# Optimization experiments

Measured on AMD Instinct MI355X. Metric: run time of the kernel, lower is better.

Reference implementation:

```python
import jax, jax.numpy as jnp
import numpy as np

B, N, F_IN = 2, 768, 10
FEATS = [F_IN, 128, 128, 64]  # DeepSet layer widths
D2 = 2 * FEATS[-1]            # lin2: cat of two broadcasts
H_MLP = 64                    # suffix hidden width
OUT = 1
SCALE = 0.05


def setup_inputs() -> dict:
    key = jax.random.key(0)
    ks = jax.random.split(key, 32)
    d = {"x": jax.random.normal(ks[0], (B, N, F_IN), dtype=jnp.float32)}
    i = 1
    for l, (ci, co) in enumerate(zip(FEATS[:-1], FEATS[1:])):
        d[f"w1_{l}"] = SCALE * jax.random.normal(ks[i], (co, ci), dtype=jnp.float32); i += 1
        d[f"b1_{l}"] = SCALE * jax.random.normal(ks[i], (co,), dtype=jnp.float32); i += 1
        d[f"w2_{l}"] = SCALE * jax.random.normal(ks[i], (co, ci), dtype=jnp.float32); i += 1
        d[f"b2_{l}"] = SCALE * jax.random.normal(ks[i], (co,), dtype=jnp.float32); i += 1
    d["sw0"] = SCALE * jax.random.normal(ks[i], (H_MLP, D2), dtype=jnp.float32); i += 1
    d["sb0"] = SCALE * jax.random.normal(ks[i], (H_MLP,), dtype=jnp.float32); i += 1
    d["sw1"] = SCALE * jax.random.normal(ks[i], (OUT, H_MLP), dtype=jnp.float32); i += 1
    d["sb1"] = SCALE * jax.random.normal(ks[i], (OUT,), dtype=jnp.float32)
    return d


def _deepset_layer(h, w1, b1, w2, b2):
    # h: (B, C, N). layer1(h) + layer2(h - mean_N(h)), both 1x1 convs.
    hm = h - h.mean(axis=2, keepdims=True)
    y = jnp.einsum('oc,bcn->bon', w1, h) + b1[None, :, None]
    y = y + jnp.einsum('oc,bcn->bon', w2, hm) + b2[None, :, None]
    return y


def reference(x, w1_0, b1_0, w2_0, b2_0, w1_1, b1_1, w2_1, b2_1,
              w1_2, b1_2, w2_2, b2_2, sw0, sb0, sw1, sb1):
    h = x.transpose(0, 2, 1)  # (B, F_IN, N)
    h = jax.nn.relu(_deepset_layer(h, w1_0, b1_0, w2_0, b2_0))
    h = jax.nn.relu(_deepset_layer(h, w1_1, b1_1, w2_1, b2_1))
    u = _deepset_layer(h, w1_2, b1_2, w2_2, b2_2)  # (B, f, N), no ReLU after last
    f = u.shape[1]
    # lin2 block: cat(m1, m2) over channels with m1[b,c,i,j]=u[b,c,j],
    # m2[b,c,i,j]=u[b,c,i]. The first 1x1 conv distributes over the concat:
    #   sw0 @ block = sw0[:, :f] @ m1 + sw0[:, f:] @ m2
    p = jnp.einsum('oc,bcn->bon', sw0[:, :f], u)   # contribution broadcast over i
    q = jnp.einsum('oc,bcn->bon', sw0[:, f:], u)   # contribution broadcast over j
    h1 = jax.nn.relu(p[:, :, None, :] + q[:, :, :, None] + sb0[None, :, None, None])  # (B, H, N, N)
    out = jnp.einsum('oc,bcij->boij', sw1, h1) + sb1[None, :, None, None]  # (B, 1, N, N)
    return out
```

## Files before the change

kernel.cpp:

```cpp
#include <hip/hip_runtime.h>

#define BB 2
#define NN 768
#define FIN 10

#define WPQ_OFF 0
#define S1P_OFF 16384
#define S2P_OFF (S1P_OFF + BB*6*128)
#define H1_OFF  (S2P_OFF + BB*12*128)
#define H2_OFF  (H1_OFF + BB*128*NN)
#define PP_OFF  (H2_OFF + BB*128*NN)
#define QQ_OFF  (PP_OFF + BB*64*NN)

__global__ void k_wpq(const float* __restrict__ sw0, const float* __restrict__ w1_2,
                      const float* __restrict__ w2_2, float* __restrict__ wpq)
{
    const int o0 = blockIdx.x * 16, tid = threadIdx.x;
    __shared__ float w2l[64][132];
    __shared__ float sl[16][64];
    for (int idx = tid; idx < 2048; idx += 256) {
        int k = idx >> 5, c4 = (idx & 31) * 4;
        float4 a = *(const float4*)&w1_2[k * 128 + c4];
        float4 b = *(const float4*)&w2_2[k * 128 + c4];
        float4 r = {a.x + b.x, a.y + b.y, a.z + b.z, a.w + b.w};
        *(float4*)&w2l[k][c4] = r;
    }
    for (int idx = tid; idx < 16 * 64; idx += 256) {
        int o = idx >> 6, k = idx & 63;
        int oo = o0 + o;
        sl[o][k] = (oo < 64) ? sw0[oo * 128 + k] : sw0[(oo - 64) * 128 + 64 + k];
    }
    __syncthreads();
    const int tx = tid & 31, ty = tid >> 5;
    float4 a0 = {0, 0, 0, 0}, a1 = {0, 0, 0, 0};
    for (int k = 0; k < 64; ++k) {
        float4 wv = *(const float4*)&w2l[k][tx * 4];
        float s0 = sl[ty * 2][k], s1 = sl[ty * 2 + 1][k];
        a0.x += s0 * wv.x; a0.y += s0 * wv.y; a0.z += s0 * wv.z; a0.w += s0 * wv.w;
        a1.x += s1 * wv.x; a1.y += s1 * wv.y; a1.z += s1 * wv.z; a1.w += s1 * wv.w;
    }
    *(float4*)&wpq[(o0 + ty * 2) * 128 + tx * 4] = a0;
    *(float4*)&wpq[(o0 + ty * 2 + 1) * 128 + tx * 4] = a1;
}

__global__ void k_layer0(const float* __restrict__ x, const float* __restrict__ w1,
                         const float* __restrict__ w2, const float* __restrict__ b1,
                         const float* __restrict__ b2, float* __restrict__ h1,
                         float* __restrict__ s1p)
{
    const int b = blockIdx.x, nblk = blockIdx.y, n0 = nblk * 128, tid = threadIdx.x;
    __shared__ float red[FIN][257];
    __shared__ float mu[FIN];
    __shared__ float xt[FIN][128];
    __shared__ float wl[FIN][128];
    __shared__ float offs[128];
    __shared__ float red2[8][16][33];
    float acc[FIN];
#pragma unroll
    for (int c = 0; c < FIN; ++c) acc[c] = 0.f;
    for (int n = tid; n < NN; n += 256) {
        const float* xp = x + (b * NN + n) * FIN;
#pragma unroll
        for (int c = 0; c < FIN; ++c) acc[c] += xp[c];
    }
#pragma unroll
    for (int c = 0; c < FIN; ++c) red[c][tid] = acc[c];
    __syncthreads();
    for (int s = 128; s > 0; s >>= 1) {
        if (tid < s) {
#pragma unroll
            for (int c = 0; c < FIN; ++c) red[c][tid] += red[c][tid + s];
        }
        __syncthreads();
    }
    if (tid < FIN) mu[tid] = red[tid][0] * (1.f / (float)NN);
    for (int idx = tid; idx < FIN * 128; idx += 256) {
        int n = idx / FIN, c = idx % FIN;
        xt[c][n] = x[(b * NN + n0 + n) * FIN + c];
    }
    for (int idx = tid; idx < FIN * 128; idx += 256) {
        int o = idx / FIN, c = idx % FIN;
        wl[c][o] = w1[o * FIN + c] + w2[o * FIN + c];
    }
    __syncthreads();
    if (tid < 128) {
        float o = b1[tid] + b2[tid];
#pragma unroll
        for (int c = 0; c < FIN; ++c) o -= w2[tid * FIN + c] * mu[c];
        offs[tid] = o;
    }
    __syncthreads();
    const int tx = tid & 31, ty = tid >> 5;
    float4 av[16];
#pragma unroll
    for (int a = 0; a < 16; ++a) {
        float o = offs[ty * 16 + a];
        av[a] = make_float4(o, o, o, o);
    }
#pragma unroll
    for (int c = 0; c < FIN; ++c) {
        float4 xv = *(const float4*)&xt[c][tx * 4];
#pragma unroll
        for (int a = 0; a < 16; ++a) {
            float w = wl[c][ty * 16 + a];
            av[a].x += w * xv.x; av[a].y += w * xv.y;
            av[a].z += w * xv.z; av[a].w += w * xv.w;
        }
    }
#pragma unroll
    for (int a = 0; a < 16; ++a) {
        float4 r = av[a];
        r.x = fmaxf(r.x, 0.f); r.y = fmaxf(r.y, 0.f);
        r.z = fmaxf(r.z, 0.f); r.w = fmaxf(r.w, 0.f);
        *(float4*)&h1[((size_t)(b * 128 + ty * 16 + a)) * NN + n0 + tx * 4] = r;
        red2[ty][a][tx] = r.x + r.y + r.z + r.w;
    }
    __syncthreads();
    if (tid < 128) {
        float s = 0.f;
#pragma unroll
        for (int t = 0; t < 32; ++t) s += red2[tid >> 4][tid & 15][t];
        s1p[(b * 6 + nblk) * 128 + tid] = s;
    }
}

__global__ void k_layer1(const float* __restrict__ h1, const float* __restrict__ w1,
                         const float* __restrict__ b1, const float* __restrict__ w2,
                         const float* __restrict__ b2, const float* __restrict__ s1p,
                         float* __restrict__ h2, float* __restrict__ s2p)
{
    const int b = blockIdx.x, nblk = blockIdx.y, n0 = nblk * 64,
              o0 = blockIdx.z * 64, tid = threadIdx.x;
    __shared__ float hl[128][64];
    __shared__ float wl[64][132];
    __shared__ float mul[128];
    __shared__ float offp[4][64];
    __shared__ float offs[64];
    __shared__ float red[16][4][17];
    if (tid < 128) {
        float s = 0.f;
#pragma unroll
        for (int k = 0; k < 6; ++k) s += s1p[(b * 6 + k) * 128 + tid];
        mul[tid] = s * (1.f / (float)NN);
    }
    for (int idx = tid; idx < 2048; idx += 256) {
        int c = idx >> 4, n4 = (idx & 15) * 4;
        *(float4*)&hl[c][n4] = *(const float4*)&h1[((size_t)(b * 128 + c)) * NN + n0 + n4];
    }
    for (int idx = tid; idx < 2048; idx += 256) {
        int o = idx >> 5, c4 = (idx & 31) * 4;
        float4 a = *(const float4*)&w1[(o0 + o) * 128 + c4];
        float4 bb = *(const float4*)&w2[(o0 + o) * 128 + c4];
        float4 r = {a.x + bb.x, a.y + bb.y, a.z + bb.z, a.w + bb.w};
        *(float4*)&wl[o][c4] = r;
    }
    __syncthreads();
    {
        int o = tid & 63, part = tid >> 6;
        const float* w2r = w2 + (o0 + o) * 128 + part * 32;
        const float* mr = mul + part * 32;
        float p = 0.f;
#pragma unroll
        for (int i = 0; i < 32; ++i) p += w2r[i] * mr[i];
        offp[part][o] = p;
    }
    __syncthreads();
    if (tid < 64)
        offs[tid] = b1[o0 + tid] + b2[o0 + tid]
                  - offp[0][tid] - offp[1][tid] - offp[2][tid] - offp[3][tid];
    __syncthreads();
    const int tx = tid & 15, ty = tid >> 4;
    float4 acc[4];
#pragma unroll
    for (int a = 0; a < 4; ++a) acc[a] = make_float4(0.f, 0.f, 0.f, 0.f);
    for (int c = 0; c < 128; ++c) {
        float4 hv = *(const float4*)&hl[c][tx * 4];
#pragma unroll
        for (int a = 0; a < 4; ++a) {
            float w = wl[ty * 4 + a][c];
            acc[a].x += w * hv.x; acc[a].y += w * hv.y;
            acc[a].z += w * hv.z; acc[a].w += w * hv.w;
        }
    }
#pragma unroll
    for (int a = 0; a < 4; ++a) {
        int o = ty * 4 + a;
        float off = offs[o];
        float4 r = acc[a];
        r.x = fmaxf(r.x + off, 0.f); r.y = fmaxf(r.y + off, 0.f);
        r.z = fmaxf(r.z + off, 0.f); r.w = fmaxf(r.w + off, 0.f);
        *(float4*)&h2[((size_t)(b * 128 + o0 + o)) * NN + n0 + tx * 4] = r;
        red[ty][a][tx] = r.x + r.y + r.z + r.w;
    }
    __syncthreads();
    if (tid < 64) {
        float s = 0.f;
#pragma unroll
        for (int t = 0; t < 16; ++t) s += red[tid >> 2][tid & 3][t];
        s2p[(b * 12 + nblk) * 128 + o0 + tid] = s;
    }
}

__global__ void k_pq(const float* __restrict__ h2, const float* __restrict__ wpq,
                     const float* __restrict__ b1_2, const float* __restrict__ w2_2,
                     const float* __restrict__ b2_2, const float* __restrict__ sw0,
                     const float* __restrict__ sb0, const float* __restrict__ s2p,
                     float* __restrict__ pp, float* __restrict__ qq)
{
    const int b = blockIdx.x, nblk = blockIdx.y, n0 = nblk * 64,
              z = blockIdx.z, o0 = z * 64, tid = threadIdx.x;
    __shared__ float hl[128][64];
    __shared__ float wl[64][132];
    __shared__ float mul[128];
    __shared__ float offp[4][64];
    __shared__ float off2[64];
    __shared__ float bp[4][64];
    __shared__ float bias[64];
    if (tid < 128) {
        float s = 0.f;
#pragma unroll
        for (int k = 0; k < 12; ++k) s += s2p[(b * 12 + k) * 128 + tid];
        mul[tid] = s * (1.f / (float)NN);
    }
    for (int idx = tid; idx < 2048; idx += 256) {
        int c = idx >> 4, n4 = (idx & 15) * 4;
        *(float4*)&hl[c][n4] = *(const float4*)&h2[((size_t)(b * 128 + c)) * NN + n0 + n4];
    }
    for (int idx = tid; idx < 2048; idx += 256) {
        int o = idx >> 5, c4 = (idx & 31) * 4;
        *(float4*)&wl[o][c4] = *(const float4*)&wpq[(o0 + o) * 128 + c4];
    }
    __syncthreads();
    {
        int k = tid & 63, part = tid >> 6;
        const float* w2r = w2_2 + k * 128 + part * 32;
        const float* mr = mul + part * 32;
        float p = 0.f;
#pragma unroll
        for (int i = 0; i < 32; ++i) p += w2r[i] * mr[i];
        offp[part][k] = p;
    }
    __syncthreads();
    if (tid < 64)
        off2[tid] = b1_2[tid] + b2_2[tid]
                  - offp[0][tid] - offp[1][tid] - offp[2][tid] - offp[3][tid];
    __syncthreads();
    {
        int o = tid & 63, part = tid >> 6;
        const float* srow = sw0 + o * 128 + (z ? 64 : 0) + part * 16;
        float p = 0.f;
#pragma unroll
        for (int i = 0; i < 16; ++i) p += srow[i] * off2[part * 16 + i];
        bp[part][o] = p;
    }
    __syncthreads();
    if (tid < 64)
        bias[tid] = bp[0][tid] + bp[1][tid] + bp[2][tid] + bp[3][tid]
                  + (z == 0 ? sb0[tid] : 0.f);
    __syncthreads();
    const int tx = tid & 15, ty = tid >> 4;
    float4 acc[4];
#pragma unroll
    for (int a = 0; a < 4; ++a) acc[a] = make_float4(0.f, 0.f, 0.f, 0.f);
    for (int c = 0; c < 128; ++c) {
        float4 hv = *(const float4*)&hl[c][tx * 4];
#pragma unroll
        for (int a = 0; a < 4; ++a) {
            float w = wl[ty * 4 + a][c];
            acc[a].x += w * hv.x; acc[a].y += w * hv.y;
            acc[a].z += w * hv.z; acc[a].w += w * hv.w;
        }
    }
    float* dst = (z == 0) ? pp : qq;
#pragma unroll
    for (int a = 0; a < 4; ++a) {
        int o = ty * 4 + a;
        float bb = bias[o];
        float4 r = acc[a];
        r.x += bb; r.y += bb; r.z += bb; r.w += bb;
        *(float4*)&dst[((size_t)(b * 64 + o)) * NN + n0 + tx * 4] = r;
    }
}

__global__ void k_final(const float* __restrict__ pp, const float* __restrict__ qq,
                        const float* __restrict__ sw1, const float* __restrict__ sb1,
                        float* __restrict__ out)
{
    const int b = blockIdx.x, i0 = blockIdx.y * 64, j0 = blockIdx.z * 64, tid = threadIdx.x;
    __shared__ float pl[64][64];
    __shared__ float ql[64][64];
    __shared__ float wl[64];
    __shared__ float sbv;
    for (int idx = tid; idx < 4096; idx += 512) {
        int c = idx >> 6, k = idx & 63;
        pl[c][k] = pp[((size_t)(b * 64 + c)) * NN + j0 + k];
        ql[c][k] = qq[((size_t)(b * 64 + c)) * NN + i0 + k];
    }
    if (tid < 64) wl[tid] = sw1[tid];
    if (tid == 0) sbv = sb1[0];
    __syncthreads();
    const int tx = tid & 15, ty = tid >> 4;
    float sb = sbv;
    float4 acc0 = {sb, sb, sb, sb}, acc1 = {sb, sb, sb, sb};
#pragma unroll 8
    for (int c = 0; c < 64; ++c) {
        float4 pv = *(const float4*)&pl[c][tx * 4];
        float q0 = ql[c][ty * 2], q1 = ql[c][ty * 2 + 1];
        float w = wl[c];
        acc0.x += w * fmaxf(pv.x + q0, 0.f);
        acc0.y += w * fmaxf(pv.y + q0, 0.f);
        acc0.z += w * fmaxf(pv.z + q0, 0.f);
        acc0.w += w * fmaxf(pv.w + q0, 0.f);
        acc1.x += w * fmaxf(pv.x + q1, 0.f);
        acc1.y += w * fmaxf(pv.y + q1, 0.f);
        acc1.z += w * fmaxf(pv.z + q1, 0.f);
        acc1.w += w * fmaxf(pv.w + q1, 0.f);
    }
    size_t base = (size_t)b * NN * NN + (size_t)(i0 + ty * 2) * NN + j0 + tx * 4;
    *(float4*)&out[base] = acc0;
    *(float4*)&out[base + NN] = acc1;
}

extern "C" void kernel_launch(void* const* d_in, const int* in_sizes, int n_in,
                              void* d_out, int out_size, void* d_ws, size_t ws_size,
                              hipStream_t stream)
{
    const float* x    = (const float*)d_in[0];
    const float* w1_0 = (const float*)d_in[1];
    const float* b1_0 = (const float*)d_in[2];
    const float* w2_0 = (const float*)d_in[3];
    const float* b2_0 = (const float*)d_in[4];
    const float* w1_1 = (const float*)d_in[5];
    const float* b1_1 = (const float*)d_in[6];
    const float* w2_1 = (const float*)d_in[7];
    const float* b2_1 = (const float*)d_in[8];
    const float* w1_2 = (const float*)d_in[9];
    const float* b1_2 = (const float*)d_in[10];
    const float* w2_2 = (const float*)d_in[11];
    const float* b2_2 = (const float*)d_in[12];
    const float* sw0  = (const float*)d_in[13];
    const float* sb0  = (const float*)d_in[14];
    const float* sw1  = (const float*)d_in[15];
    const float* sb1  = (const float*)d_in[16];

    float* ws   = (float*)d_ws;
    float* wpq  = ws + WPQ_OFF;
    float* s1p  = ws + S1P_OFF;
    float* s2p  = ws + S2P_OFF;
    float* h1   = ws + H1_OFF;
    float* h2   = ws + H2_OFF;
    float* pp   = ws + PP_OFF;
    float* qq   = ws + QQ_OFF;

    k_wpq   <<<8, 256, 0, stream>>>(sw0, w1_2, w2_2, wpq);
    k_layer0<<<dim3(BB, 6), 256, 0, stream>>>(x, w1_0, w2_0, b1_0, b2_0, h1, s1p);
    k_layer1<<<dim3(BB, 12, 2), 256, 0, stream>>>(h1, w1_1, b1_1, w2_1, b2_1, s1p, h2, s2p);
    k_pq    <<<dim3(BB, 12, 2), 256, 0, stream>>>(h2, wpq, b1_2, w2_2, b2_2, sw0, sb0, s2p, pp, qq);
    k_final <<<dim3(BB, 12, 12), 512, 0, stream>>>(pp, qq, sw1, sb1, (float*)d_out);
}
```

Baseline: 52.85 us.

## Fuse all stages into one persistent kernel with grid-wide atomic barriers

Replaces five separate kernel launches with a single 288-block kernel. The stages are separated by software grid barriers built from atomic counters, which are reset by a memset before each launch. Work is re-tiled into smaller N tiles (32 columns) so more blocks take part in the DeepSet layers, and the final stage uses 256 threads with 4x4 outputs per thread. The aim is to remove launch gaps and underfilled grids, at the cost of spin-wait barriers that assume all 288 blocks are resident at once, plus an extra memset.

```diff
diff --git a/kernel.cpp b/kernel.cpp
--- a/kernel.cpp
+++ b/kernel.cpp
@@ -3,322 +3,359 @@
 #define BB 2
 #define NN 768
 #define FIN 10
+#define NBLK 288
 
 #define WPQ_OFF 0
 #define S1P_OFF 16384
-#define S2P_OFF (S1P_OFF + BB*6*128)
-#define H1_OFF  (S2P_OFF + BB*12*128)
+#define S2P_OFF (S1P_OFF + BB*24*128)
+#define CTR_OFF (S2P_OFF + BB*24*128)
+#define H1_OFF  32768
 #define H2_OFF  (H1_OFF + BB*128*NN)
 #define PP_OFF  (H2_OFF + BB*128*NN)
 #define QQ_OFF  (PP_OFF + BB*64*NN)
 
-__global__ void k_wpq(const float* __restrict__ sw0, const float* __restrict__ w1_2,
-                      const float* __restrict__ w2_2, float* __restrict__ wpq)
+struct SM_L0 {
+    float xt[FIN][36];
+    float wl[FIN][128];
+    float mu[FIN];
+    float offs[128];
+    float wred[4][FIN];
+    float cred[128][9];
+};
+struct SM_L12 {
+    float hl[128][36];
+    float wl[64][132];
+    float mul[128];
+    float offp[4][64];
+    float offs[64];
+    float off2[64];
+    float bp[4][64];
+    float bias[64];
+    float cred[64][9];
+};
+struct SM_WPQ {
+    float w2l[64][132];
+    float sl[16][68];
+};
+struct SM_FIN {
+    float pl[64][68];
+    float ql[64][68];
+    float wv[64];
+    float sb;
+};
+union alignas(16) SMem { SM_L0 l0; SM_L12 l12; SM_WPQ w; SM_FIN f; };
+
+__device__ __forceinline__ void gbar(unsigned* sync, int which)
 {
-    const int o0 = blockIdx.x * 16, tid = threadIdx.x;
-    __shared__ float w2l[64][132];
-    __shared__ float sl[16][64];
-    for (int idx = tid; idx < 2048; idx += 256) {
-        int k = idx >> 5, c4 = (idx & 31) * 4;
-        float4 a = *(const float4*)&w1_2[k * 128 + c4];
-        float4 b = *(const float4*)&w2_2[k * 128 + c4];
-        float4 r = {a.x + b.x, a.y + b.y, a.z + b.z, a.w + b.w};
-        *(float4*)&w2l[k][c4] = r;
-    }
-    for (int idx = tid; idx < 16 * 64; idx += 256) {
-        int o = idx >> 6, k = idx & 63;
-        int oo = o0 + o;
-        sl[o][k] = (oo < 64) ? sw0[oo * 128 + k] : sw0[(oo - 64) * 128 + 64 + k];
-    }
     __syncthreads();
-    const int tx = tid & 31, ty = tid >> 5;
-    float4 a0 = {0, 0, 0, 0}, a1 = {0, 0, 0, 0};
-    for (int k = 0; k < 64; ++k) {
-        float4 wv = *(const float4*)&w2l[k][tx * 4];
-        float s0 = sl[ty * 2][k], s1 = sl[ty * 2 + 1][k];
-        a0.x += s0 * wv.x; a0.y += s0 * wv.y; a0.z += s0 * wv.z; a0.w += s0 * wv.w;
-        a1.x += s1 * wv.x; a1.y += s1 * wv.y; a1.z += s1 * wv.z; a1.w += s1 * wv.w;
-    }
-    *(float4*)&wpq[(o0 + ty * 2) * 128 + tx * 4] = a0;
-    *(float4*)&wpq[(o0 + ty * 2 + 1) * 128 + tx * 4] = a1;
+    if (threadIdx.x == 0) {
+        __threadfence();
+        unsigned pos = atomicAdd(&sync[which * 8], 1u);
+        if (pos == (unsigned)(NBLK - 1)) {
+            __hip_atomic_store(&sync[which * 8 + 4], 1u, __ATOMIC_RELEASE,
+                               __HIP_MEMORY_SCOPE_AGENT);
+        } else {
+            while (__hip_atomic_load(&sync[which * 8 + 4], __ATOMIC_ACQUIRE,
+                                     __HIP_MEMORY_SCOPE_AGENT) == 0u)
+                __builtin_amdgcn_s_sleep(2);
+        }
+        __threadfence();
+    }
+    __syncthreads();
 }
 
-__global__ void k_layer0(const float* __restrict__ x, const float* __restrict__ w1,
-                         const float* __restrict__ w2, const float* __restrict__ b1,
-                         const float* __restrict__ b2, float* __restrict__ h1,
-                         float* __restrict__ s1p)
+__global__ __launch_bounds__(256) void k_mega(
+    const float* __restrict__ x,
+    const float* __restrict__ w1_0, const float* __restrict__ b1_0,
+    const float* __restrict__ w2_0, const float* __restrict__ b2_0,
+    const float* __restrict__ w1_1, const float* __restrict__ b1_1,
+    const float* __restrict__ w2_1, const float* __restrict__ b2_1,
+    const float* __restrict__ w1_2, const float* __restrict__ b1_2,
+    const float* __restrict__ w2_2, const float* __restrict__ b2_2,
+    const float* __restrict__ sw0, const float* __restrict__ sb0,
+    const float* __restrict__ sw1, const float* __restrict__ sb1,
+    float* ws, float* __restrict__ out)
 {
-    const int b = blockIdx.x, nblk = blockIdx.y, n0 = nblk * 128, tid = threadIdx.x;
-    __shared__ float red[FIN][257];
-    __shared__ float mu[FIN];
-    __shared__ float xt[FIN][128];
-    __shared__ float wl[FIN][128];
-    __shared__ float offs[128];
-    __shared__ float red2[8][16][33];
-    float acc[FIN];
-#pragma unroll
-    for (int c = 0; c < FIN; ++c) acc[c] = 0.f;
-    for (int n = tid; n < NN; n += 256) {
-        const float* xp = x + (b * NN + n) * FIN;
-#pragma unroll
-        for (int c = 0; c < FIN; ++c) acc[c] += xp[c];
-    }
-#pragma unroll
-    for (int c = 0; c < FIN; ++c) red[c][tid] = acc[c];
-    __syncthreads();
-    for (int s = 128; s > 0; s >>= 1) {
-        if (tid < s) {
-#pragma unroll
-            for (int c = 0; c < FIN; ++c) red[c][tid] += red[c][tid + s];
-        }
-        __syncthreads();
-    }
-    if (tid < FIN) mu[tid] = red[tid][0] * (1.f / (float)NN);
-    for (int idx = tid; idx < FIN * 128; idx += 256) {
-        int n = idx / FIN, c = idx % FIN;
-        xt[c][n] = x[(b * NN + n0 + n) * FIN + c];
-    }
-    for (int idx = tid; idx < FIN * 128; idx += 256) {
-        int o = idx / FIN, c = idx % FIN;
-        wl[c][o] = w1[o * FIN + c] + w2[o * FIN + c];
-    }
-    __syncthreads();
-    if (tid < 128) {
-        float o = b1[tid] + b2[tid];
-#pragma unroll
-        for (int c = 0; c < FIN; ++c) o -= w2[tid * FIN + c] * mu[c];
-        offs[tid] = o;
-    }
-    __syncthreads();
-    const int tx = tid & 31, ty = tid >> 5;
-    float4 av[16];
-#pragma unroll
-    for (int a = 0; a < 16; ++a) {
-        float o = offs[ty * 16 + a];
-        av[a] = make_float4(o, o, o, o);
-    }
-#pragma unroll
-    for (int c = 0; c < FIN; ++c) {
-        float4 xv = *(const float4*)&xt[c][tx * 4];
-#pragma unroll
-        for (int a = 0; a < 16; ++a) {
-            float w = wl[c][ty * 16 + a];
-            av[a].x += w * xv.x; av[a].y += w * xv.y;
-            av[a].z += w * xv.z; av[a].w += w * xv.w;
-        }
-    }
-#pragma unroll
-    for (int a = 0; a < 16; ++a) {
-        float4 r = av[a];
-        r.x = fmaxf(r.x, 0.f); r.y = fmaxf(r.y, 0.f);
-        r.z = fmaxf(r.z, 0.f); r.w = fmaxf(r.w, 0.f);
-        *(float4*)&h1[((size_t)(b * 128 + ty * 16 + a)) * NN + n0 + tx * 4] = r;
-        red2[ty][a][tx] = r.x + r.y + r.z + r.w;
-    }
-    __syncthreads();
-    if (tid < 128) {
-        float s = 0.f;
-#pragma unroll
-        for (int t = 0; t < 32; ++t) s += red2[tid >> 4][tid & 15][t];
-        s1p[(b * 6 + nblk) * 128 + tid] = s;
-    }
-}
-
-__global__ void k_layer1(const float* __restrict__ h1, const float* __restrict__ w1,
-                         const float* __restrict__ b1, const float* __restrict__ w2,
-                         const float* __restrict__ b2, const float* __restrict__ s1p,
-                         float* __restrict__ h2, float* __restrict__ s2p)
-{
-    const int b = blockIdx.x, nblk = blockIdx.y, n0 = nblk * 64,
-              o0 = blockIdx.z * 64, tid = threadIdx.x;
-    __shared__ float hl[128][64];
-    __shared__ float wl[64][132];
-    __shared__ float mul[128];
-    __shared__ float offp[4][64];
-    __shared__ float offs[64];
-    __shared__ float red[16][4][17];
-    if (tid < 128) {
-        float s = 0.f;
-#pragma unroll
-        for (int k = 0; k < 6; ++k) s += s1p[(b * 6 + k) * 128 + tid];
-        mul[tid] = s * (1.f / (float)NN);
-    }
-    for (int idx = tid; idx < 2048; idx += 256) {
-        int c = idx >> 4, n4 = (idx & 15) * 4;
-        *(float4*)&hl[c][n4] = *(const float4*)&h1[((size_t)(b * 128 + c)) * NN + n0 + n4];
-    }
-    for (int idx = tid; idx < 2048; idx += 256) {
-        int o = idx >> 5, c4 = (idx & 31) * 4;
-        float4 a = *(const float4*)&w1[(o0 + o) * 128 + c4];
-        float4 bb = *(const float4*)&w2[(o0 + o) * 128 + c4];
-        float4 r = {a.x + bb.x, a.y + bb.y, a.z + bb.z, a.w + bb.w};
-        *(float4*)&wl[o][c4] = r;
-    }
-    __syncthreads();
+    __shared__ SMem sm;
+    const int blk = blockIdx.x, tid = threadIdx.x;
+
+    float* wpq = ws + WPQ_OFF;
+    float* s1p = ws + S1P_OFF;
+    float* s2p = ws + S2P_OFF;
+    float* h1  = ws + H1_OFF;
+    float* h2  = ws + H2_OFF;
+    float* pp  = ws + PP_OFF;
+    float* qq  = ws + QQ_OFF;
+    unsigned* sync = (unsigned*)(ws + CTR_OFF);
+
+    if (blk < 48) {
+        const int b = blk / 24, nt = blk % 24, n0 = nt * 32;
+        for (int idx = tid; idx < FIN * 32; idx += 256) {
+            int n = idx / FIN, c = idx % FIN;
+            sm.l0.xt[c][n] = x[(b * NN + n0 + n) * FIN + c];
+        }
+        for (int idx = tid; idx < FIN * 128; idx += 256) {
+            int o = idx / FIN, c = idx % FIN;
+            sm.l0.wl[c][o] = w1_0[o * FIN + c] + w2_0[o * FIN + c];
+        }
+        float part[FIN];
+#pragma unroll
+        for (int c = 0; c < FIN; ++c) part[c] = 0.f;
+        for (int n = tid; n < NN; n += 256) {
+            const float* xp = x + (b * NN + n) * FIN;
+#pragma unroll
+            for (int c = 0; c < FIN; ++c) part[c] += xp[c];
+        }
+#pragma unroll
+        for (int off = 32; off > 0; off >>= 1) {
+#pragma unroll
+            for (int c = 0; c < FIN; ++c) part[c] += __shfl_down(part[c], off);
+        }
+        if ((tid & 63) == 0) {
+#pragma unroll
+            for (int c = 0; c < FIN; ++c) sm.l0.wred[tid >> 6][c] = part[c];
+        }
+        __syncthreads();
+        if (tid < FIN) {
+            float s = sm.l0.wred[0][tid] + sm.l0.wred[1][tid]
+                    + sm.l0.wred[2][tid] + sm.l0.wred[3][tid];
+            sm.l0.mu[tid] = s * (1.f / (float)NN);
+        }
+        __syncthreads();
+        if (tid < 128) {
+            float o = b1_0[tid] + b2_0[tid];
+#pragma unroll
+            for (int c = 0; c < FIN; ++c) o -= w2_0[tid * FIN + c] * sm.l0.mu[c];
+            sm.l0.offs[tid] = o;
+        }
+        __syncthreads();
+        const int tx = tid & 7, ty = tid >> 3;
+        float4 acc[4];
+#pragma unroll
+        for (int a = 0; a < 4; ++a) {
+            float o = sm.l0.offs[ty * 4 + a];
+            acc[a] = make_float4(o, o, o, o);
+        }
+#pragma unroll
+        for (int c = 0; c < FIN; ++c) {
+            float4 xv = *(const float4*)&sm.l0.xt[c][tx * 4];
+#pragma unroll
+            for (int a = 0; a < 4; ++a) {
+                float w = sm.l0.wl[c][ty * 4 + a];
+                acc[a].x += w * xv.x; acc[a].y += w * xv.y;
+                acc[a].z += w * xv.z; acc[a].w += w * xv.w;
+            }
+        }
+#pragma unroll
+        for (int a = 0; a < 4; ++a) {
+            int o = ty * 4 + a;
+            float4 r = acc[a];
+            r.x = fmaxf(r.x, 0.f); r.y = fmaxf(r.y, 0.f);
+            r.z = fmaxf(r.z, 0.f); r.w = fmaxf(r.w, 0.f);
+            *(float4*)&h1[((size_t)(b * 128 + o)) * NN + n0 + tx * 4] = r;
+            sm.l0.cred[o][tx] = r.x + r.y + r.z + r.w;
+        }
+        __syncthreads();
+        if (tid < 128) {
+            float s = 0.f;
+#pragma unroll
+            for (int t = 0; t < 8; ++t) s += sm.l0.cred[tid][t];
+            s1p[(b * 24 + nt) * 128 + tid] = s;
+        }
+    } else if (blk >= 280) {
+        const int o0 = (blk - 280) * 16;
+        for (int idx = tid; idx < 2048; idx += 256) {
+            int k = idx >> 5, c4 = (idx & 31) * 4;
+            float4 a = *(const float4*)&w1_2[k * 128 + c4];
+            float4 b = *(const float4*)&w2_2[k * 128 + c4];
+            float4 r = {a.x + b.x, a.y + b.y, a.z + b.z, a.w + b.w};
+            *(float4*)&sm.w.w2l[k][c4] = r;
+        }
+        for (int idx = tid; idx < 16 * 64; idx += 256) {
+            int o = idx >> 6, k = idx & 63;
+            int oo = o0 + o;
+            sm.w.sl[o][k] = (oo < 64) ? sw0[oo * 128 + k] : sw0[(oo - 64) * 128 + 64 + k];
+        }
+        __syncthreads();
+        const int tx = tid & 31, ty = tid >> 5;
+        float4 a0 = {0, 0, 0, 0}, a1 = {0, 0, 0, 0};
+        for (int k = 0; k < 64; ++k) {
+            float4 wv = *(const float4*)&sm.w.w2l[k][tx * 4];
+            float s0 = sm.w.sl[ty * 2][k], s1v = sm.w.sl[ty * 2 + 1][k];
+            a0.x += s0 * wv.x; a0.y += s0 * wv.y; a0.z += s0 * wv.z; a0.w += s0 * wv.w;
+            a1.x += s1v * wv.x; a1.y += s1v * wv.y; a1.z += s1v * wv.z; a1.w += s1v * wv.w;
+        }
+        *(float4*)&wpq[(o0 + ty * 2) * 128 + tx * 4] = a0;
+        *(float4*)&wpq[(o0 + ty * 2 + 1) * 128 + tx * 4] = a1;
+    }
+    gbar(sync, 0);
+
+    if (blk < 96) {
+        const int b = blk & 1, z = (blk >> 1) & 1, nt = blk >> 2;
+        const int n0 = nt * 32, o0 = z * 64;
+        if (tid < 128) {
+            float s = 0.f;
+#pragma unroll
+            for (int k = 0; k < 24; ++k) s += s1p[(b * 24 + k) * 128 + tid];
+            sm.l12.mul[tid] = s * (1.f / (float)NN);
+        }
+        for (int idx = tid; idx < 1024; idx += 256) {
+            int c = idx >> 3, n4 = (idx & 7) * 4;
+            *(float4*)&sm.l12.hl[c][n4] = *(const float4*)&h1[((size_t)(b * 128 + c)) * NN + n0 + n4];
+        }
+        for (int idx = tid; idx < 2048; idx += 256) {
+            int o = idx >> 5, c4 = (idx & 31) * 4;
+            float4 a = *(const float4*)&w1_1[(o0 + o) * 128 + c4];
+            float4 bb = *(const float4*)&w2_1[(o0 + o) * 128 + c4];
+            float4 r = {a.x + bb.x, a.y + bb.y, a.z + bb.z, a.w + bb.w};
+            *(float4*)&sm.l12.wl[o][c4] = r;
+        }
+        __syncthreads();
+        {
+            int o = tid & 63, p = tid >> 6;
+            const float* w2r = w2_1 + (o0 + o) * 128 + p * 32;
+            const float* mr = sm.l12.mul + p * 32;
+            float s = 0.f;
+#pragma unroll
+            for (int i = 0; i < 32; ++i) s += w2r[i] * mr[i];
+            sm.l12.offp[p][o] = s;
+        }
+        __syncthreads();
+        if (tid < 64)
+            sm.l12.offs[tid] = b1_1[o0 + tid] + b2_1[o0 + tid]
+                             - sm.l12.offp[0][tid] - sm.l12.offp[1][tid]
+                             - sm.l12.offp[2][tid] - sm.l12.offp[3][tid];
+        __syncthreads();
+        const int tx = tid & 7, ty = tid >> 3;
+        float4 a0 = {0, 0, 0, 0}, a1 = {0, 0, 0, 0};
+        for (int c = 0; c < 128; ++c) {
+            float4 hv = *(const float4*)&sm.l12.hl[c][tx * 4];
+            float w0 = sm.l12.wl[ty * 2][c], w1v = sm.l12.wl[ty * 2 + 1][c];
+            a0.x += w0 * hv.x; a0.y += w0 * hv.y; a0.z += w0 * hv.z; a0.w += w0 * hv.w;
+            a1.x += w1v * hv.x; a1.y += w1v * hv.y; a1.z += w1v * hv.z; a1.w += w1v * hv.w;
+        }
+#pragma unroll
+        for (int a = 0; a < 2; ++a) {
+            int o = ty * 2 + a;
+            float off = sm.l12.offs[o];
+            float4 r = a ? a1 : a0;
+            r.x = fmaxf(r.x + off, 0.f); r.y = fmaxf(r.y + off, 0.f);
+            r.z = fmaxf(r.z + off, 0.f); r.w = fmaxf(r.w + off, 0.f);
+            *(float4*)&h2[((size_t)(b * 128 + o0 + o)) * NN + n0 + tx * 4] = r;
+            sm.l12.cred[o][tx] = r.x + r.y + r.z + r.w;
+        }
+        __syncthreads();
+        if (tid < 64) {
+            float s = 0.f;
+#pragma unroll
+            for (int t = 0; t < 8; ++t) s += sm.l12.cred[tid][t];
+            s2p[(b * 24 + nt) * 128 + o0 + tid] = s;
+        }
+    }
+    gbar(sync, 1);
+
+    if (blk < 96) {
+        const int b = blk & 1, z = (blk >> 1) & 1, nt = blk >> 2;
+        const int n0 = nt * 32, o0 = z * 64;
+        if (tid < 128) {
+            float s = 0.f;
+#pragma unroll
+            for (int k = 0; k < 24; ++k) s += s2p[(b * 24 + k) * 128 + tid];
+            sm.l12.mul[tid] = s * (1.f / (float)NN);
+        }
+        for (int idx = tid; idx < 1024; idx += 256) {
+            int c = idx >> 3, n4 = (idx & 7) * 4;
+            *(float4*)&sm.l12.hl[c][n4] = *(const float4*)&h2[((size_t)(b * 128 + c)) * NN + n0 + n4];
+        }
+        for (int idx = tid; idx < 2048; idx += 256) {
+            int o = idx >> 5, c4 = (idx & 31) * 4;
+            *(float4*)&sm.l12.wl[o][c4] = *(const float4*)&wpq[(o0 + o) * 128 + c4];
+        }
+        __syncthreads();
+        {
+            int k = tid & 63, p = tid >> 6;
+            const float* w2r = w2_2 + k * 128 + p * 32;
+            const float* mr = sm.l12.mul + p * 32;
+            float s = 0.f;
+#pragma unroll
+            for (int i = 0; i < 32; ++i) s += w2r[i] * mr[i];
+            sm.l12.offp[p][k] = s;
+        }
+        __syncthreads();
+        if (tid < 64)
+            sm.l12.off2[tid] = b1_2[tid] + b2_2[tid]
+                             - sm.l12.offp[0][tid] - sm.l12.offp[1][tid]
+                             - sm.l12.offp[2][tid] - sm.l12.offp[3][tid];
+        __syncthreads();
+        {
+            int o = tid & 63, p = tid >> 6;
+            const float* srow = sw0 + o * 128 + (z ? 64 : 0) + p * 16;
+            float s = 0.f;
+#pragma unroll
+            for (int i = 0; i < 16; ++i) s += srow[i] * sm.l12.off2[p * 16 + i];
+            sm.l12.bp[p][o] = s;
+        }
+        __syncthreads();
+        if (tid < 64)
+            sm.l12.bias[tid] = sm.l12.bp[0][tid] + sm.l12.bp[1][tid]
+                             + sm.l12.bp[2][tid] + sm.l12.bp[3][tid]
+                             + (z == 0 ? sb0[tid] : 0.f);
+        __syncthreads();
+        const int tx = tid & 7, ty = tid >> 3;
+        float4 a0 = {0, 0, 0, 0}, a1 = {0, 0, 0, 0};
+        for (int c = 0; c < 128; ++c) {
+            float4 hv = *(const float4*)&sm.l12.hl[c][tx * 4];
+            float w0 = sm.l12.wl[ty * 2][c], w1v = sm.l12.wl[ty * 2 + 1][c];
+            a0.x += w0 * hv.x; a0.y += w0 * hv.y; a0.z += w0 * hv.z; a0.w += w0 * hv.w;
+            a1.x += w1v * hv.x; a1.y += w1v * hv.y; a1.z += w1v * hv.z; a1.w += w1v * hv.w;
+        }
+        float* dst = (z == 0) ? pp : qq;
+#pragma unroll
+        for (int a = 0; a < 2; ++a) {
+            int o = ty * 2 + a;
+            float bb = sm.l12.bias[o];
+            float4 r = a ? a1 : a0;
+            r.x += bb; r.y += bb; r.z += bb; r.w += bb;
+            *(float4*)&dst[((size_t)(b * 64 + o)) * NN + n0 + tx * 4] = r;
+        }
+    }
+    gbar(sync, 2);
+
     {
-        int o = tid & 63, part = tid >> 6;
-        const float* w2r = w2 + (o0 + o) * 128 + part * 32;
-        const float* mr = mul + part * 32;
-        float p = 0.f;
-#pragma unroll
-        for (int i = 0; i < 32; ++i) p += w2r[i] * mr[i];
-        offp[part][o] = p;
-    }
-    __syncthreads();
-    if (tid < 64)
-        offs[tid] = b1[o0 + tid] + b2[o0 + tid]
-                  - offp[0][tid] - offp[1][tid] - offp[2][tid] - offp[3][tid];
-    __syncthreads();
-    const int tx = tid & 15, ty = tid >> 4;
-    float4 acc[4];
-#pragma unroll
-    for (int a = 0; a < 4; ++a) acc[a] = make_float4(0.f, 0.f, 0.f, 0.f);
-    for (int c = 0; c < 128; ++c) {
-        float4 hv = *(const float4*)&hl[c][tx * 4];
+        const int b = blk / 144, rem = blk % 144;
+        const int i0 = (rem / 12) * 64, j0 = (rem % 12) * 64;
+        for (int idx = tid; idx < 1024; idx += 256) {
+            int c = idx >> 4, k4 = (idx & 15) * 4;
+            *(float4*)&sm.f.pl[c][k4] = *(const float4*)&pp[((size_t)(b * 64 + c)) * NN + j0 + k4];
+            *(float4*)&sm.f.ql[c][k4] = *(const float4*)&qq[((size_t)(b * 64 + c)) * NN + i0 + k4];
+        }
+        if (tid < 64) sm.f.wv[tid] = sw1[tid];
+        if (tid == 0) sm.f.sb = sb1[0];
+        __syncthreads();
+        const int tx = tid & 15, ty = tid >> 4;
+        float sb = sm.f.sb;
+        float4 acc[4];
+#pragma unroll
+        for (int a = 0; a < 4; ++a) acc[a] = make_float4(sb, sb, sb, sb);
+#pragma unroll 4
+        for (int c = 0; c < 64; ++c) {
+            float4 pv = *(const float4*)&sm.f.pl[c][tx * 4];
+            float w = sm.f.wv[c];
+#pragma unroll
+            for (int a = 0; a < 4; ++a) {
+                float qv = sm.f.ql[c][ty * 4 + a];
+                acc[a].x += w * fmaxf(pv.x + qv, 0.f);
+                acc[a].y += w * fmaxf(pv.y + qv, 0.f);
+                acc[a].z += w * fmaxf(pv.z + qv, 0.f);
+                acc[a].w += w * fmaxf(pv.w + qv, 0.f);
+            }
+        }
 #pragma unroll
         for (int a = 0; a < 4; ++a) {
-            float w = wl[ty * 4 + a][c];
-            acc[a].x += w * hv.x; acc[a].y += w * hv.y;
-            acc[a].z += w * hv.z; acc[a].w += w * hv.w;
-        }
-    }
-#pragma unroll
-    for (int a = 0; a < 4; ++a) {
-        int o = ty * 4 + a;
-        float off = offs[o];
-        float4 r = acc[a];
-        r.x = fmaxf(r.x + off, 0.f); r.y = fmaxf(r.y + off, 0.f);
-        r.z = fmaxf(r.z + off, 0.f); r.w = fmaxf(r.w + off, 0.f);
-        *(float4*)&h2[((size_t)(b * 128 + o0 + o)) * NN + n0 + tx * 4] = r;
-        red[ty][a][tx] = r.x + r.y + r.z + r.w;
-    }
-    __syncthreads();
-    if (tid < 64) {
-        float s = 0.f;
-#pragma unroll
-        for (int t = 0; t < 16; ++t) s += red[tid >> 2][tid & 3][t];
-        s2p[(b * 12 + nblk) * 128 + o0 + tid] = s;
-    }
-}
-
-__global__ void k_pq(const float* __restrict__ h2, const float* __restrict__ wpq,
-                     const float* __restrict__ b1_2, const float* __restrict__ w2_2,
-                     const float* __restrict__ b2_2, const float* __restrict__ sw0,
-                     const float* __restrict__ sb0, const float* __restrict__ s2p,
-                     float* __restrict__ pp, float* __restrict__ qq)
-{
-    const int b = blockIdx.x, nblk = blockIdx.y, n0 = nblk * 64,
-              z = blockIdx.z, o0 = z * 64, tid = threadIdx.x;
-    __shared__ float hl[128][64];
-    __shared__ float wl[64][132];
-    __shared__ float mul[128];
-    __shared__ float offp[4][64];
-    __shared__ float off2[64];
-    __shared__ float bp[4][64];
-    __shared__ float bias[64];
-    if (tid < 128) {
-        float s = 0.f;
-#pragma unroll
-        for (int k = 0; k < 12; ++k) s += s2p[(b * 12 + k) * 128 + tid];
-        mul[tid] = s * (1.f / (float)NN);
-    }
-    for (int idx = tid; idx < 2048; idx += 256) {
-        int c = idx >> 4, n4 = (idx & 15) * 4;
-        *(float4*)&hl[c][n4] = *(const float4*)&h2[((size_t)(b * 128 + c)) * NN + n0 + n4];
-    }
-    for (int idx = tid; idx < 2048; idx += 256) {
-        int o = idx >> 5, c4 = (idx & 31) * 4;
-        *(float4*)&wl[o][c4] = *(const float4*)&wpq[(o0 + o) * 128 + c4];
-    }
-    __syncthreads();
-    {
-        int k = tid & 63, part = tid >> 6;
-        const float* w2r = w2_2 + k * 128 + part * 32;
-        const float* mr = mul + part * 32;
-        float p = 0.f;
-#pragma unroll
-        for (int i = 0; i < 32; ++i) p += w2r[i] * mr[i];
-        offp[part][k] = p;
-    }
-    __syncthreads();
-    if (tid < 64)
-        off2[tid] = b1_2[tid] + b2_2[tid]
-                  - offp[0][tid] - offp[1][tid] - offp[2][tid] - offp[3][tid];
-    __syncthreads();
-    {
-        int o = tid & 63, part = tid >> 6;
-        const float* srow = sw0 + o * 128 + (z ? 64 : 0) + part * 16;
-        float p = 0.f;
-#pragma unroll
-        for (int i = 0; i < 16; ++i) p += srow[i] * off2[part * 16 + i];
-        bp[part][o] = p;
-    }
-    __syncthreads();
-    if (tid < 64)
-        bias[tid] = bp[0][tid] + bp[1][tid] + bp[2][tid] + bp[3][tid]
-                  + (z == 0 ? sb0[tid] : 0.f);
-    __syncthreads();
-    const int tx = tid & 15, ty = tid >> 4;
-    float4 acc[4];
-#pragma unroll
-    for (int a = 0; a < 4; ++a) acc[a] = make_float4(0.f, 0.f, 0.f, 0.f);
-    for (int c = 0; c < 128; ++c) {
-        float4 hv = *(const float4*)&hl[c][tx * 4];
-#pragma unroll
-        for (int a = 0; a < 4; ++a) {
-            float w = wl[ty * 4 + a][c];
-            acc[a].x += w * hv.x; acc[a].y += w * hv.y;
-            acc[a].z += w * hv.z; acc[a].w += w * hv.w;
-        }
-    }
-    float* dst = (z == 0) ? pp : qq;
-#pragma unroll
-    for (int a = 0; a < 4; ++a) {
-        int o = ty * 4 + a;
-        float bb = bias[o];
-        float4 r = acc[a];
-        r.x += bb; r.y += bb; r.z += bb; r.w += bb;
-        *(float4*)&dst[((size_t)(b * 64 + o)) * NN + n0 + tx * 4] = r;
-    }
-}
-
-__global__ void k_final(const float* __restrict__ pp, const float* __restrict__ qq,
-                        const float* __restrict__ sw1, const float* __restrict__ sb1,
-                        float* __restrict__ out)
-{
-    const int b = blockIdx.x, i0 = blockIdx.y * 64, j0 = blockIdx.z * 64, tid = threadIdx.x;
-    __shared__ float pl[64][64];
-    __shared__ float ql[64][64];
-    __shared__ float wl[64];
-    __shared__ float sbv;
-    for (int idx = tid; idx < 4096; idx += 512) {
-        int c = idx >> 6, k = idx & 63;
-        pl[c][k] = pp[((size_t)(b * 64 + c)) * NN + j0 + k];
-        ql[c][k] = qq[((size_t)(b * 64 + c)) * NN + i0 + k];
-    }
-    if (tid < 64) wl[tid] = sw1[tid];
-    if (tid == 0) sbv = sb1[0];
-    __syncthreads();
-    const int tx = tid & 15, ty = tid >> 4;
-    float sb = sbv;
-    float4 acc0 = {sb, sb, sb, sb}, acc1 = {sb, sb, sb, sb};
-#pragma unroll 8
-    for (int c = 0; c < 64; ++c) {
-        float4 pv = *(const float4*)&pl[c][tx * 4];
-        float q0 = ql[c][ty * 2], q1 = ql[c][ty * 2 + 1];
-        float w = wl[c];
-        acc0.x += w * fmaxf(pv.x + q0, 0.f);
-        acc0.y += w * fmaxf(pv.y + q0, 0.f);
-        acc0.z += w * fmaxf(pv.z + q0, 0.f);
-        acc0.w += w * fmaxf(pv.w + q0, 0.f);
-        acc1.x += w * fmaxf(pv.x + q1, 0.f);
-        acc1.y += w * fmaxf(pv.y + q1, 0.f);
-        acc1.z += w * fmaxf(pv.z + q1, 0.f);
-        acc1.w += w * fmaxf(pv.w + q1, 0.f);
-    }
-    size_t base = (size_t)b * NN * NN + (size_t)(i0 + ty * 2) * NN + j0 + tx * 4;
-    *(float4*)&out[base] = acc0;
-    *(float4*)&out[base + NN] = acc1;
+            size_t base = (size_t)b * NN * NN + (size_t)(i0 + ty * 4 + a) * NN + j0 + tx * 4;
+            *(float4*)&out[base] = acc[a];
+        }
+    }
 }
 
 extern "C" void kernel_launch(void* const* d_in, const int* in_sizes, int n_in,
@@ -343,18 +380,12 @@
     const float* sw1  = (const float*)d_in[15];
     const float* sb1  = (const float*)d_in[16];
 
-    float* ws   = (float*)d_ws;
-    float* wpq  = ws + WPQ_OFF;
-    float* s1p  = ws + S1P_OFF;
-    float* s2p  = ws + S2P_OFF;
-    float* h1   = ws + H1_OFF;
-    float* h2   = ws + H2_OFF;
-    float* pp   = ws + PP_OFF;
-    float* qq   = ws + QQ_OFF;
-
-    k_wpq   <<<8, 256, 0, stream>>>(sw0, w1_2, w2_2, wpq);
-    k_layer0<<<dim3(BB, 6), 256, 0, stream>>>(x, w1_0, w2_0, b1_0, b2_0, h1, s1p);
-    k_layer1<<<dim3(BB, 12, 2), 256, 0, stream>>>(h1, w1_1, b1_1, w2_1, b2_1, s1p, h2, s2p);
-    k_pq    <<<dim3(BB, 12, 2), 256, 0, stream>>>(h2, wpq, b1_2, w2_2, b2_2, sw0, sb0, s2p, pp, qq);
-    k_final <<<dim3(BB, 12, 12), 512, 0, stream>>>(pp, qq, sw1, sb1, (float*)d_out);
+    float* ws = (float*)d_ws;
+
+    (void)hipMemsetAsync(ws + CTR_OFF, 0, 24 * sizeof(unsigned), stream);
+
+    k_mega<<<dim3(NBLK), 256, 0, stream>>>(
+        x, w1_0, b1_0, w2_0, b2_0, w1_1, b1_1, w2_1, b2_1,
+        w1_2, b1_2, w2_2, b2_2, sw0, sb0, sw1, sb1,
+        ws, (float*)d_out);
 }
```

After: 176.2 us. 3.33x slower.
